# Optimization experiments

Hardware: AMD Instinct MI355X
Metric: run time of the kernel (lower is better)

The kernel has to match this reference:

```python
import jax, jax.numpy as jnp
import numpy as np

B, LI, LC, H = 16, 2048, 2048, 1024


def setup_inputs() -> dict:
    key = jax.random.key(0)
    k1, k2, k3, k4 = jax.random.split(key, 4)
    inp = jax.random.normal(k1, (B, LI, H), dtype=jnp.float32)
    ctx = jax.random.normal(k2, (B, LC, H), dtype=jnp.float32)
    # mask out the last quarter of context positions (True = masked), never a full row
    context_mask = jnp.broadcast_to(jnp.arange(LC) >= (3 * LC) // 4, (B, LC))
    W = jax.random.normal(k3, (H, H), dtype=jnp.float32) * (1.0 / np.sqrt(H))
    b = jax.random.normal(k4, (H,), dtype=jnp.float32) * 0.01
    return {"input": inp, "context": ctx, "context_mask": context_mask, "W": W, "b": b}


def reference(input, context, context_mask, W, b):
    # shared relu-projected linear for query and key/value sides
    q = jax.nn.relu(jnp.einsum('bih,oh->bio', input, W) + b)    # [B, Li, H]
    k = jax.nn.relu(jnp.einsum('bjh,oh->bjo', context, W) + b)  # [B, Lc, H]
    scores = jnp.einsum('bid,bjd->bij', q, k)                    # [B, Li, Lc], no scaling
    scores = jnp.where(context_mask[:, None, :], -jnp.inf, scores)
    probs = jax.nn.softmax(scores, axis=2)
    return jnp.einsum('bij,bjd->bid', probs, k)                  # weighted sum of context hiddens
```

## Files before the change

### kernel.cpp

```cpp
#include <hip/hip_runtime.h>

typedef _Float16 half8 __attribute__((ext_vector_type(8)));
typedef _Float16 half4 __attribute__((ext_vector_type(4)));
typedef float floatx4 __attribute__((ext_vector_type(4)));

#define OFF_X    0L
#define OFF_S    0L
#define OFF_P    67108864L
#define OFF_W    134217728L
#define OFF_QK   136314880L
#define OFF_KT   270532608L
#define OFF_MASK 337641472L
#define WS_NEED  337674240L

__device__ __forceinline__ void glds16(const void* g, void* l) {
  __builtin_amdgcn_global_load_lds(
      (__attribute__((address_space(1))) void*)(void*)(g),
      (__attribute__((address_space(3))) void*)(l), 16, 0, 0);
}

__global__ void mask_canon(const unsigned* __restrict__ raw,
                           unsigned char* __restrict__ outm) {
  __shared__ int flag;
  int t = threadIdx.x;
  if (t == 0) flag = 0;
  __syncthreads();
  int loc = 0;
  for (int i = t; i < 8192; i += 256)
    if (raw[i] > 1u) loc = 1;
  if (loc) flag = 1;
  __syncthreads();
  if (flag) {
    const unsigned char* b8 = (const unsigned char*)raw;
    for (int j = t; j < 32768; j += 256) outm[j] = (b8[j] != 0);
  } else {
    const int* r32 = (const int*)raw;
    for (int j = t; j < 32768; j += 256) outm[j] = (r32[j] != 0);
  }
}

__global__ __launch_bounds__(256) void cvt_f32_f16(const float* __restrict__ x,
                                                   _Float16* __restrict__ y, long n) {
  long i = ((long)blockIdx.x * 256 + threadIdx.x) * 4;
  if (i + 3 < n) {
    float4 v = *(const float4*)(x + i);
    half4 h;
    h[0] = (_Float16)v.x; h[1] = (_Float16)v.y;
    h[2] = (_Float16)v.z; h[3] = (_Float16)v.w;
    *(half4*)(y + i) = h;
  }
}

template <bool EPI>
__global__ __launch_bounds__(256, 3)
void gemm_nt(const _Float16* __restrict__ A, long sAz,
             const _Float16* __restrict__ B, long sBz,
             void* __restrict__ Cv, long sCz,
             const float* __restrict__ bias, int K, int ldc) {
  __shared__ _Float16 As[128 * 64];
  __shared__ _Float16 Bs[128 * 64];
  const int t = threadIdx.x;
  const int l = t & 63;
  const int w = t >> 6;
  A += (long)blockIdx.z * sAz + (long)blockIdx.y * 128 * K;
  B += (long)blockIdx.z * sBz + (long)blockIdx.x * 128 * K;
  const int waveM = (w >> 1) * 64, waveN = (w & 1) * 64;
  const int l15 = l & 15, quad = l >> 4;
  const int srow = l >> 3;
  const int gchunk = (l & 7) ^ (srow & 7);

  floatx4 acc[4][4] = {};

  for (int kt = 0; kt < K; kt += 64) {
    __syncthreads();
#pragma unroll
    for (int c = 0; c < 4; c++) {
      const int r = w * 32 + c * 8;
      glds16(A + (long)(r + srow) * K + kt + gchunk * 8, As + r * 64);
      glds16(B + (long)(r + srow) * K + kt + gchunk * 8, Bs + r * 64);
    }
    __syncthreads();
#pragma unroll
    for (int k32 = 0; k32 < 2; k32++) {
      half8 af[4], bfr[4];
#pragma unroll
      for (int mi = 0; mi < 4; mi++) {
        const int r = waveM + mi * 16 + l15;
        const int cc = (k32 * 4 + quad) ^ (r & 7);
        af[mi] = *(const half8*)(As + r * 64 + cc * 8);
      }
#pragma unroll
      for (int ni = 0; ni < 4; ni++) {
        const int r = waveN + ni * 16 + l15;
        const int cc = (k32 * 4 + quad) ^ (r & 7);
        bfr[ni] = *(const half8*)(Bs + r * 64 + cc * 8);
      }
#pragma unroll
      for (int mi = 0; mi < 4; mi++)
#pragma unroll
        for (int ni = 0; ni < 4; ni++)
          acc[mi][ni] = __builtin_amdgcn_mfma_f32_16x16x32_f16(af[mi], bfr[ni],
                                                               acc[mi][ni], 0, 0, 0);
    }
  }

  const int rowb = quad * 4;
  if constexpr (EPI) {
    _Float16* Cp = (_Float16*)Cv + (long)blockIdx.z * sCz +
                   (long)blockIdx.y * 128 * ldc + blockIdx.x * 128;
#pragma unroll
    for (int mi = 0; mi < 4; mi++)
#pragma unroll
      for (int ni = 0; ni < 4; ni++) {
        const int col = waveN + ni * 16 + l15;
        const float bv = bias[blockIdx.x * 128 + col];
#pragma unroll
        for (int p = 0; p < 4; p++) {
          const int row = waveM + mi * 16 + rowb + p;
          Cp[(long)row * ldc + col] = (_Float16)fmaxf(acc[mi][ni][p] + bv, 0.f);
        }
      }
  } else {
    float* Cp = (float*)Cv + (long)blockIdx.z * sCz +
                (long)blockIdx.y * 128 * ldc + blockIdx.x * 128;
#pragma unroll
    for (int mi = 0; mi < 4; mi++)
#pragma unroll
      for (int ni = 0; ni < 4; ni++) {
        const int col = waveN + ni * 16 + l15;
#pragma unroll
        for (int p = 0; p < 4; p++) {
          const int row = waveM + mi * 16 + rowb + p;
          Cp[(long)row * ldc + col] = acc[mi][ni][p];
        }
      }
  }
}

__global__ __launch_bounds__(256) void transpose_k(const _Float16* __restrict__ Km,
                                                   _Float16* __restrict__ KT) {
  __shared__ _Float16 tile[64 * 72];
  const int t = threadIdx.x;
  const long b = blockIdx.z;
  const _Float16* src = Km + (b * 2048 + blockIdx.x * 64) * 1024 + blockIdx.y * 64;
  {
    const int jl = t >> 2, hc = (t & 3) * 16;
    half8 v0 = *(const half8*)(src + (long)jl * 1024 + hc);
    half8 v1 = *(const half8*)(src + (long)jl * 1024 + hc + 8);
    *(half8*)&tile[jl * 72 + hc] = v0;
    *(half8*)&tile[jl * 72 + hc + 8] = v1;
  }
  __syncthreads();
  {
    const int hl = t >> 2, jc = (t & 3) * 16;
    half8 o0, o1;
#pragma unroll
    for (int jj = 0; jj < 8; jj++) o0[jj] = tile[(jc + jj) * 72 + hl];
#pragma unroll
    for (int jj = 0; jj < 8; jj++) o1[jj] = tile[(jc + 8 + jj) * 72 + hl];
    long off = (b * 1024 + blockIdx.y * 64 + hl) * 2048 + blockIdx.x * 64 + jc;
    *(half8*)(KT + off) = o0;
    *(half8*)(KT + off + 8) = o1;
  }
}

__global__ __launch_bounds__(256) void softmax_k(const float* __restrict__ S,
                                                 _Float16* __restrict__ P,
                                                 const unsigned char* __restrict__ mask,
                                                 int b0) {
  const int i = blockIdx.x, z = blockIdx.y, t = threadIdx.x;
  const float* s = S + ((long)z * 2048 + i) * 2048;
  const unsigned char* mrow = mask + (long)(b0 + z) * 2048;
  const int base0 = t * 4, base1 = 1024 + t * 4;
  float4 a0 = *(const float4*)(s + base0);
  float4 a1 = *(const float4*)(s + base1);
  float v[8] = {a0.x, a0.y, a0.z, a0.w, a1.x, a1.y, a1.z, a1.w};
  const float NINF = -__builtin_inff();
#pragma unroll
  for (int k = 0; k < 4; k++) {
    if (mrow[base0 + k]) v[k] = NINF;
    if (mrow[base1 + k]) v[4 + k] = NINF;
  }
  float mx = v[0];
#pragma unroll
  for (int k = 1; k < 8; k++) mx = fmaxf(mx, v[k]);
#pragma unroll
  for (int o = 32; o >= 1; o >>= 1) mx = fmaxf(mx, __shfl_xor(mx, o, 64));
  __shared__ float redm[4], reds[4];
  if ((t & 63) == 0) redm[t >> 6] = mx;
  __syncthreads();
  mx = fmaxf(fmaxf(redm[0], redm[1]), fmaxf(redm[2], redm[3]));
  float e[8], sm = 0.f;
#pragma unroll
  for (int k = 0; k < 8; k++) { e[k] = __expf(v[k] - mx); sm += e[k]; }
#pragma unroll
  for (int o = 32; o >= 1; o >>= 1) sm += __shfl_xor(sm, o, 64);
  if ((t & 63) == 0) reds[t >> 6] = sm;
  __syncthreads();
  sm = reds[0] + reds[1] + reds[2] + reds[3];
  const float inv = 1.0f / sm;
  _Float16* p = P + ((long)z * 2048 + i) * 2048;
  half4 h0, h1;
#pragma unroll
  for (int k = 0; k < 4; k++) { h0[k] = (_Float16)(e[k] * inv); h1[k] = (_Float16)(e[4 + k] * inv); }
  *(half4*)(p + base0) = h0;
  *(half4*)(p + base1) = h1;
}

extern "C" void kernel_launch(void* const* d_in, const int* in_sizes, int n_in,
                              void* d_out, int out_size, void* d_ws, size_t ws_size,
                              hipStream_t stream) {
  (void)in_sizes; (void)n_in; (void)out_size;
  if ((long)ws_size < WS_NEED) return;

  const float* inp  = (const float*)d_in[0];
  const float* ctx  = (const float*)d_in[1];
  const unsigned* msk = (const unsigned*)d_in[2];
  const float* W    = (const float*)d_in[3];
  const float* bias = (const float*)d_in[4];
  float* out = (float*)d_out;
  char* ws = (char*)d_ws;

  _Float16* Xf   = (_Float16*)(ws + OFF_X);
  float*    Sb   = (float*)(ws + OFF_S);
  _Float16* Pb   = (_Float16*)(ws + OFF_P);
  _Float16* Wf   = (_Float16*)(ws + OFF_W);
  _Float16* QK   = (_Float16*)(ws + OFF_QK);
  _Float16* KT   = (_Float16*)(ws + OFF_KT);
  unsigned char* Mc = (unsigned char*)(ws + OFF_MASK);

  mask_canon<<<1, 256, 0, stream>>>(msk, Mc);
  cvt_f32_f16<<<32768, 256, 0, stream>>>(inp, Xf, 33554432L);
  cvt_f32_f16<<<32768, 256, 0, stream>>>(ctx, Xf + 33554432L, 33554432L);
  cvt_f32_f16<<<1024, 256, 0, stream>>>(W, Wf, 1048576L);
  gemm_nt<true><<<dim3(8, 512, 1), 256, 0, stream>>>(Xf, 0L, Wf, 0L, (void*)QK, 0L,
                                                     bias, 1024, 1024);
  transpose_k<<<dim3(32, 16, 16), 256, 0, stream>>>(QK + 32768L * 1024, KT);
  for (int bp = 0; bp < 4; bp++) {
    const _Float16* Aq = QK + (long)bp * 4 * 2048 * 1024;
    const _Float16* Bk = QK + (32768L + (long)bp * 4 * 2048) * 1024;
    gemm_nt<false><<<dim3(16, 16, 4), 256, 0, stream>>>(Aq, 2048L * 1024, Bk, 2048L * 1024,
                                                        (void*)Sb, 2048L * 2048, nullptr,
                                                        1024, 2048);
    softmax_k<<<dim3(2048, 4), 256, 0, stream>>>(Sb, Pb, Mc, bp * 4);
    gemm_nt<false><<<dim3(8, 16, 4), 256, 0, stream>>>(Pb, 2048L * 2048,
                                                       KT + (long)bp * 4 * 1024 * 2048,
                                                       1024L * 2048,
                                                       (void*)(out + (long)bp * 4 * 2048 * 1024),
                                                       2048L * 1024, nullptr, 2048, 1024);
  }
}
```

Measured before the change: 1.039 ms.

## Skip fully masked context tiles and fuse fp32-to-fp16 conversion into projection GEMM

Builds per-64-column flags marking context blocks that are entirely masked. The scores GEMM skips output tiles that are fully masked, and the PV GEMM skips K-steps over them. Softmax avoids reading those scores and writing their probabilities. Separately, the projection GEMM now reads fp32 inputs directly and converts them to fp16 in registers, which removes the two large conversion passes and their fp16 intermediate buffer. The mask-dependent skipping is general and correct for any mask, though in the PV GEMM the skip branch sits before __syncthreads, which is safe only because the flag is uniform across the block.

```diff
diff --git a/kernel.cpp b/kernel.cpp
--- a/kernel.cpp
+++ b/kernel.cpp
@@ -4,14 +4,14 @@
 typedef _Float16 half4 __attribute__((ext_vector_type(4)));
 typedef float floatx4 __attribute__((ext_vector_type(4)));
 
-#define OFF_X    0L
 #define OFF_S    0L
 #define OFF_P    67108864L
+#define OFF_MASK 100663296L
+#define OFF_FLAGS 100696064L
 #define OFF_W    134217728L
 #define OFF_QK   136314880L
 #define OFF_KT   270532608L
-#define OFF_MASK 337641472L
-#define WS_NEED  337674240L
+#define WS_NEED  337641472L
 
 __device__ __forceinline__ void glds16(const void* g, void* l) {
   __builtin_amdgcn_global_load_lds(
@@ -20,7 +20,8 @@
 }
 
 __global__ void mask_canon(const unsigned* __restrict__ raw,
-                           unsigned char* __restrict__ outm) {
+                           unsigned char* __restrict__ outm,
+                           unsigned char* __restrict__ flags) {
   __shared__ int flag;
   int t = threadIdx.x;
   if (t == 0) flag = 0;
@@ -36,6 +37,13 @@
   } else {
     const int* r32 = (const int*)raw;
     for (int j = t; j < 32768; j += 256) outm[j] = (r32[j] != 0);
+  }
+  __syncthreads();
+  for (int c = t; c < 512; c += 256) {
+    const unsigned char* p = outm + c * 64;
+    unsigned char all = 1;
+    for (int k = 0; k < 64; k++) all &= p[k];
+    flags[c] = all;
   }
 }
 
@@ -51,14 +59,94 @@
   }
 }
 
-template <bool EPI>
+__global__ __launch_bounds__(256, 3)
+void gemm_proj(const float* __restrict__ Ainp, const float* __restrict__ Actx,
+               const _Float16* __restrict__ Bw, _Float16* __restrict__ C,
+               const float* __restrict__ bias) {
+  __shared__ __align__(16) _Float16 As[128 * 64];
+  __shared__ __align__(16) _Float16 Bs[128 * 64];
+  const int t = threadIdx.x, l = t & 63, w = t >> 6;
+  const float* A = (blockIdx.y < 256) ? Ainp : Actx;
+  A += (long)(blockIdx.y & 255) * 128 * 1024;
+  const _Float16* B = Bw + (long)blockIdx.x * 128 * 1024;
+  const int waveM = (w >> 1) * 64, waveN = (w & 1) * 64;
+  const int l15 = l & 15, quad = l >> 4;
+  const int srow = l >> 3;
+  const int gcol = (l & 7) * 8;
+  const int gchunkB = (l & 7) ^ (srow & 7);
+
+  floatx4 acc[4][4] = {};
+
+  for (int kt = 0; kt < 1024; kt += 64) {
+    __syncthreads();
+#pragma unroll
+    for (int c = 0; c < 4; c++) {
+      const int rb = w * 32 + c * 8;
+      glds16(B + (long)(rb + srow) * 1024 + kt + gchunkB * 8, Bs + rb * 64);
+      const int ra = rb + srow;
+      float4 v0 = *(const float4*)(A + (long)ra * 1024 + kt + gcol);
+      float4 v1 = *(const float4*)(A + (long)ra * 1024 + kt + gcol + 4);
+      half8 h;
+      h[0] = (_Float16)v0.x; h[1] = (_Float16)v0.y;
+      h[2] = (_Float16)v0.z; h[3] = (_Float16)v0.w;
+      h[4] = (_Float16)v1.x; h[5] = (_Float16)v1.y;
+      h[6] = (_Float16)v1.z; h[7] = (_Float16)v1.w;
+      const int ch = (l & 7) ^ (ra & 7);
+      *(half8*)(As + ra * 64 + ch * 8) = h;
+    }
+    __syncthreads();
+#pragma unroll
+    for (int k32 = 0; k32 < 2; k32++) {
+      half8 af[4], bfr[4];
+#pragma unroll
+      for (int mi = 0; mi < 4; mi++) {
+        const int r = waveM + mi * 16 + l15;
+        const int cc = (k32 * 4 + quad) ^ (r & 7);
+        af[mi] = *(const half8*)(As + r * 64 + cc * 8);
+      }
+#pragma unroll
+      for (int ni = 0; ni < 4; ni++) {
+        const int r = waveN + ni * 16 + l15;
+        const int cc = (k32 * 4 + quad) ^ (r & 7);
+        bfr[ni] = *(const half8*)(Bs + r * 64 + cc * 8);
+      }
+#pragma unroll
+      for (int mi = 0; mi < 4; mi++)
+#pragma unroll
+        for (int ni = 0; ni < 4; ni++)
+          acc[mi][ni] = __builtin_amdgcn_mfma_f32_16x16x32_f16(af[mi], bfr[ni],
+                                                               acc[mi][ni], 0, 0, 0);
+    }
+  }
+
+  const int rowb = quad * 4;
+  _Float16* Cp = C + (long)blockIdx.y * 128 * 1024 + blockIdx.x * 128;
+#pragma unroll
+  for (int mi = 0; mi < 4; mi++)
+#pragma unroll
+    for (int ni = 0; ni < 4; ni++) {
+      const int col = waveN + ni * 16 + l15;
+      const float bv = bias[blockIdx.x * 128 + col];
+#pragma unroll
+      for (int p = 0; p < 4; p++) {
+        const int row = waveM + mi * 16 + rowb + p;
+        Cp[(long)row * 1024 + col] = (_Float16)fmaxf(acc[mi][ni][p] + bv, 0.f);
+      }
+    }
+}
+
+template <int MODE>
 __global__ __launch_bounds__(256, 3)
 void gemm_nt(const _Float16* __restrict__ A, long sAz,
              const _Float16* __restrict__ B, long sBz,
-             void* __restrict__ Cv, long sCz,
-             const float* __restrict__ bias, int K, int ldc) {
-  __shared__ _Float16 As[128 * 64];
-  __shared__ _Float16 Bs[128 * 64];
+             float* __restrict__ Cv, long sCz,
+             const unsigned char* __restrict__ jflags, int K, int ldc) {
+  if (MODE == 1) {
+    const unsigned char* f = jflags + blockIdx.z * 32 + blockIdx.x * 2;
+    if (f[0] & f[1]) return;
+  }
+  __shared__ __align__(16) _Float16 As[128 * 64];
+  __shared__ __align__(16) _Float16 Bs[128 * 64];
   const int t = threadIdx.x;
   const int l = t & 63;
   const int w = t >> 6;
@@ -72,6 +160,9 @@
   floatx4 acc[4][4] = {};
 
   for (int kt = 0; kt < K; kt += 64) {
+    if (MODE == 2) {
+      if (jflags[blockIdx.z * 32 + (kt >> 6)]) continue;
+    }
     __syncthreads();
 #pragma unroll
     for (int c = 0; c < 4; c++) {
@@ -105,36 +196,19 @@
   }
 
   const int rowb = quad * 4;
-  if constexpr (EPI) {
-    _Float16* Cp = (_Float16*)Cv + (long)blockIdx.z * sCz +
-                   (long)blockIdx.y * 128 * ldc + blockIdx.x * 128;
-#pragma unroll
-    for (int mi = 0; mi < 4; mi++)
-#pragma unroll
-      for (int ni = 0; ni < 4; ni++) {
-        const int col = waveN + ni * 16 + l15;
-        const float bv = bias[blockIdx.x * 128 + col];
-#pragma unroll
-        for (int p = 0; p < 4; p++) {
-          const int row = waveM + mi * 16 + rowb + p;
-          Cp[(long)row * ldc + col] = (_Float16)fmaxf(acc[mi][ni][p] + bv, 0.f);
-        }
-      }
-  } else {
-    float* Cp = (float*)Cv + (long)blockIdx.z * sCz +
-                (long)blockIdx.y * 128 * ldc + blockIdx.x * 128;
-#pragma unroll
-    for (int mi = 0; mi < 4; mi++)
-#pragma unroll
-      for (int ni = 0; ni < 4; ni++) {
-        const int col = waveN + ni * 16 + l15;
-#pragma unroll
-        for (int p = 0; p < 4; p++) {
-          const int row = waveM + mi * 16 + rowb + p;
-          Cp[(long)row * ldc + col] = acc[mi][ni][p];
-        }
-      }
-  }
+  float* Cp = Cv + (long)blockIdx.z * sCz +
+              (long)blockIdx.y * 128 * ldc + blockIdx.x * 128;
+#pragma unroll
+  for (int mi = 0; mi < 4; mi++)
+#pragma unroll
+    for (int ni = 0; ni < 4; ni++) {
+      const int col = waveN + ni * 16 + l15;
+#pragma unroll
+      for (int p = 0; p < 4; p++) {
+        const int row = waveM + mi * 16 + rowb + p;
+        Cp[(long)row * ldc + col] = acc[mi][ni][p];
+      }
+    }
 }
 
 __global__ __launch_bounds__(256) void transpose_k(const _Float16* __restrict__ Km,
@@ -167,19 +241,30 @@
 __global__ __launch_bounds__(256) void softmax_k(const float* __restrict__ S,
                                                  _Float16* __restrict__ P,
                                                  const unsigned char* __restrict__ mask,
+                                                 const unsigned char* __restrict__ flags,
                                                  int b0) {
   const int i = blockIdx.x, z = blockIdx.y, t = threadIdx.x;
   const float* s = S + ((long)z * 2048 + i) * 2048;
   const unsigned char* mrow = mask + (long)(b0 + z) * 2048;
+  const unsigned char* frow = flags + (long)(b0 + z) * 32;
   const int base0 = t * 4, base1 = 1024 + t * 4;
-  float4 a0 = *(const float4*)(s + base0);
-  float4 a1 = *(const float4*)(s + base1);
-  float v[8] = {a0.x, a0.y, a0.z, a0.w, a1.x, a1.y, a1.z, a1.w};
+  const bool f0 = frow[base0 >> 6] != 0;
+  const bool f1 = frow[base1 >> 6] != 0;
   const float NINF = -__builtin_inff();
-#pragma unroll
-  for (int k = 0; k < 4; k++) {
-    if (mrow[base0 + k]) v[k] = NINF;
-    if (mrow[base1 + k]) v[4 + k] = NINF;
+  float v[8] = {NINF, NINF, NINF, NINF, NINF, NINF, NINF, NINF};
+  if (!f0) {
+    float4 a0 = *(const float4*)(s + base0);
+    v[0] = a0.x; v[1] = a0.y; v[2] = a0.z; v[3] = a0.w;
+#pragma unroll
+    for (int k = 0; k < 4; k++)
+      if (mrow[base0 + k]) v[k] = NINF;
+  }
+  if (!f1) {
+    float4 a1 = *(const float4*)(s + base1);
+    v[4] = a1.x; v[5] = a1.y; v[6] = a1.z; v[7] = a1.w;
+#pragma unroll
+    for (int k = 0; k < 4; k++)
+      if (mrow[base1 + k]) v[4 + k] = NINF;
   }
   float mx = v[0];
 #pragma unroll
@@ -200,11 +285,18 @@
   sm = reds[0] + reds[1] + reds[2] + reds[3];
   const float inv = 1.0f / sm;
   _Float16* p = P + ((long)z * 2048 + i) * 2048;
-  half4 h0, h1;
-#pragma unroll
-  for (int k = 0; k < 4; k++) { h0[k] = (_Float16)(e[k] * inv); h1[k] = (_Float16)(e[4 + k] * inv); }
-  *(half4*)(p + base0) = h0;
-  *(half4*)(p + base1) = h1;
+  if (!f0) {
+    half4 h0;
+#pragma unroll
+    for (int k = 0; k < 4; k++) h0[k] = (_Float16)(e[k] * inv);
+    *(half4*)(p + base0) = h0;
+  }
+  if (!f1) {
+    half4 h1;
+#pragma unroll
+    for (int k = 0; k < 4; k++) h1[k] = (_Float16)(e[4 + k] * inv);
+    *(half4*)(p + base1) = h1;
+  }
 }
 
 extern "C" void kernel_launch(void* const* d_in, const int* in_sizes, int n_in,
@@ -221,32 +313,29 @@
   float* out = (float*)d_out;
   char* ws = (char*)d_ws;
 
-  _Float16* Xf   = (_Float16*)(ws + OFF_X);
   float*    Sb   = (float*)(ws + OFF_S);
   _Float16* Pb   = (_Float16*)(ws + OFF_P);
   _Float16* Wf   = (_Float16*)(ws + OFF_W);
   _Float16* QK   = (_Float16*)(ws + OFF_QK);
   _Float16* KT   = (_Float16*)(ws + OFF_KT);
   unsigned char* Mc = (unsigned char*)(ws + OFF_MASK);
-
-  mask_canon<<<1, 256, 0, stream>>>(msk, Mc);
-  cvt_f32_f16<<<32768, 256, 0, stream>>>(inp, Xf, 33554432L);
-  cvt_f32_f16<<<32768, 256, 0, stream>>>(ctx, Xf + 33554432L, 33554432L);
+  unsigned char* Fl = (unsigned char*)(ws + OFF_FLAGS);
+
+  mask_canon<<<1, 256, 0, stream>>>(msk, Mc, Fl);
   cvt_f32_f16<<<1024, 256, 0, stream>>>(W, Wf, 1048576L);
-  gemm_nt<true><<<dim3(8, 512, 1), 256, 0, stream>>>(Xf, 0L, Wf, 0L, (void*)QK, 0L,
-                                                     bias, 1024, 1024);
+  gemm_proj<<<dim3(8, 512, 1), 256, 0, stream>>>(inp, ctx, Wf, QK, bias);
   transpose_k<<<dim3(32, 16, 16), 256, 0, stream>>>(QK + 32768L * 1024, KT);
   for (int bp = 0; bp < 4; bp++) {
     const _Float16* Aq = QK + (long)bp * 4 * 2048 * 1024;
     const _Float16* Bk = QK + (32768L + (long)bp * 4 * 2048) * 1024;
-    gemm_nt<false><<<dim3(16, 16, 4), 256, 0, stream>>>(Aq, 2048L * 1024, Bk, 2048L * 1024,
-                                                        (void*)Sb, 2048L * 2048, nullptr,
-                                                        1024, 2048);
-    softmax_k<<<dim3(2048, 4), 256, 0, stream>>>(Sb, Pb, Mc, bp * 4);
-    gemm_nt<false><<<dim3(8, 16, 4), 256, 0, stream>>>(Pb, 2048L * 2048,
-                                                       KT + (long)bp * 4 * 1024 * 2048,
-                                                       1024L * 2048,
-                                                       (void*)(out + (long)bp * 4 * 2048 * 1024),
-                                                       2048L * 1024, nullptr, 2048, 1024);
-  }
-}
+    const unsigned char* Fq = Fl + bp * 4 * 32;
+    gemm_nt<1><<<dim3(16, 16, 4), 256, 0, stream>>>(Aq, 2048L * 1024, Bk, 2048L * 1024,
+                                                    Sb, 2048L * 2048, Fq, 1024, 2048);
+    softmax_k<<<dim3(2048, 4), 256, 0, stream>>>(Sb, Pb, Mc, Fl, bp * 4);
+    gemm_nt<2><<<dim3(8, 16, 4), 256, 0, stream>>>(Pb, 2048L * 2048,
+                                                   KT + (long)bp * 4 * 1024 * 2048,
+                                                   1024L * 2048,
+                                                   out + (long)bp * 4 * 2048 * 1024,
+                                                   2048L * 1024, Fq, 2048, 1024);
+  }
+}
```

New measurement: 1.127 ms. 1.08x slower.
